# Performance work log

Hardware: AMD Instinct MI355X
Metric: run time of the kernel (lower is better)

## Reference

```python
import math
import jax, jax.numpy as jnp
import numpy as np

H = 16  # num_heads

def get_alibi_slopes(n):
    def pow2_slopes(n):
        start = 2 ** (-2 ** (-(math.log2(n) - 3)))
        return [start * start ** i for i in range(n)]
    if math.log2(n).is_integer():
        return pow2_slopes(n)
    c = 2 ** math.floor(math.log2(n))
    return pow2_slopes(c) + get_alibi_slopes(2 * c)[0::2][: n - c]

def alibi_bias(num_heads, L, dtype=jnp.float32):
    slopes = jnp.asarray(get_alibi_slopes(num_heads), dtype=dtype)  # [H]
    pos = jnp.arange(L)
    rel = (pos[None, :] - pos[:, None]).astype(dtype)               # [L, L] = x - y
    bias = slopes[:, None, None] * rel[None, :, :]                  # [H, L, L]
    causal = pos[None, :] <= pos[:, None]                           # tril mask
    return jnp.where(causal[None, :, :], bias, -jnp.inf)


def setup_inputs() -> dict:
    key = jax.random.key(0)
    ks = jax.random.split(key, 4)
    D = 1024
    B, L = 2, 2048
    s_in = 1.0 / math.sqrt(D)
    return {
        "x": jax.random.normal(ks[0], (B, L, D), dtype=jnp.float32),
        "w_in": jax.random.normal(ks[1], (D, 3 * D), dtype=jnp.float32) * s_in,
        "b_in": jnp.zeros((3 * D,), dtype=jnp.float32),
        "w_out": jax.random.normal(ks[2], (D, D), dtype=jnp.float32) * s_in,
        "b_out": jnp.zeros((D,), dtype=jnp.float32),
    }


def reference(x, w_in, b_in, w_out, b_out):
    B, L, D = x.shape
    dh = D // H
    qkv = x @ w_in + b_in                                   # [B, L, 3D]
    q, k, v = jnp.split(qkv, 3, axis=-1)
    # [B, L, D] -> [B, H, L, dh]
    def heads(t):
        return t.reshape(B, L, H, dh).transpose(0, 2, 1, 3)
    q, k, v = heads(q), heads(k), heads(v)
    scores = jnp.einsum("bhqd,bhkd->bhqk", q, k) / math.sqrt(dh)
    scores = scores + alibi_bias(H, L, scores.dtype)[None]  # [B, H, L, L]
    attn = jax.nn.softmax(scores, axis=-1)
    out = jnp.einsum("bhqk,bhkd->bhqd", attn, v)            # [B, H, L, dh]
    out = out.transpose(0, 2, 1, 3).reshape(B, L, D)
    return out @ w_out + b_out
```

## Files before the change

kernel.cpp:

```cpp
#include <hip/hip_runtime.h>
#include <stdint.h>
#include <math.h>

#define NH 16
#define DH 64
#define SEQ 2048
#define DMODEL 1024

typedef short short8 __attribute__((ext_vector_type(8)));
typedef short short4v __attribute__((ext_vector_type(4)));
typedef float f32x4 __attribute__((ext_vector_type(4)));
typedef __bf16 bf16x4 __attribute__((ext_vector_type(4)));

__device__ __forceinline__ short f2bf(float f) {
  __bf16 h = (__bf16)f;
  return __builtin_bit_cast(short, h);
}
__device__ __forceinline__ short4v cvt4(f32x4 v) {
  bf16x4 b = __builtin_convertvector(v, bf16x4);
  return __builtin_bit_cast(short4v, b);
}
__device__ __forceinline__ float fast_exp2(float x) {
#if __has_builtin(__builtin_amdgcn_exp2f)
  return __builtin_amdgcn_exp2f(x);
#else
  return exp2f(x);
#endif
}

typedef const __attribute__((address_space(1))) uint32_t* gp_t;
typedef __attribute__((address_space(3))) uint32_t* lp_t;
__device__ __forceinline__ void async16(const short* g, short* l) {
  __builtin_amdgcn_global_load_lds((gp_t)g, (lp_t)l, 16, 0, 0);
}

__device__ __forceinline__ void transpose_tile(const float* __restrict__ in,
                                               short* __restrict__ out, int R, int C,
                                               int t, int tilesX, int tid) {
  __shared__ float tile[32][33];
  const int tx = tid & 31, ty = tid >> 5;
  const int c0 = (t % tilesX) * 32, r0 = (t / tilesX) * 32;
#pragma unroll
  for (int i = 0; i < 4; ++i)
    tile[ty + i * 8][tx] = in[(size_t)(r0 + ty + i * 8) * C + c0 + tx];
  __syncthreads();
#pragma unroll
  for (int i = 0; i < 4; ++i)
    out[(size_t)(c0 + ty + i * 8) * R + r0 + tx] = f2bf(tile[tx][ty + i * 8]);
}

__global__ void k_prep(const float* __restrict__ x, short* __restrict__ xb,
                       const float* __restrict__ w_in, short* __restrict__ w_in_t,
                       const float* __restrict__ w_out, short* __restrict__ w_out_t) {
  const int tid = threadIdx.x;
  const int blk = blockIdx.x;
  if (blk < 4096) {
    const int i = blk * 256 + tid;
    f32x4 v = ((const f32x4*)x)[i];
    ((short4v*)xb)[i] = cvt4(v);
  } else if (blk < 4096 + 3072) {
    transpose_tile(w_in, w_in_t, 1024, 3072, blk - 4096, 96, tid);
  } else {
    transpose_tile(w_out, w_out_t, 1024, 1024, blk - 7168, 32, tid);
  }
}

template <int MODE>
__launch_bounds__(256, 3)
__global__ void k_gemm(const short* __restrict__ A, const short* __restrict__ Bt,
                       const float* __restrict__ bias, float* __restrict__ Cf,
                       short* __restrict__ qo, short* __restrict__ ko,
                       short* __restrict__ vo) {
  constexpr int KD = 1024;
  __shared__ __align__(16) short As[128 * 64];
  __shared__ __align__(16) short Bs[128 * 64];
  const int tid = threadIdx.x;
  const int wave = tid >> 6, lane = tid & 63;
  const int quad = lane >> 4, l16 = lane & 15;
  const int wm = wave >> 1, wn = wave & 1;
  const int tM = blockIdx.y * 128, tN = blockIdx.x * 128;

  const short* pA[4];
  const short* pB[4];
  short* lA[4];
  short* lB[4];
#pragma unroll
  for (int t = 0; t < 4; ++t) {
    const int c = t * 256 + tid;
    const int row = c >> 3, gch = (c & 7) ^ (row & 7);
    pA[t] = A + (size_t)(tM + row) * KD + gch * 8;
    pB[t] = Bt + (size_t)(tN + row) * KD + gch * 8;
    lA[t] = &As[c * 8];
    lB[t] = &Bs[c * 8];
  }

  const int sw = l16 & 7;
  const int col0 = (quad ^ sw) << 3;
  const int col1 = col0 ^ 32;

  f32x4 acc[4][4] = {};

  for (int k0 = 0; k0 < KD; k0 += 64) {
    __syncthreads();
#pragma unroll
    for (int t = 0; t < 4; ++t) {
      async16(pA[t] + k0, lA[t]);
      async16(pB[t] + k0, lB[t]);
    }
    __syncthreads();
#pragma unroll
    for (int kh = 0; kh < 2; ++kh) {
      const int col = kh ? col1 : col0;
      short8 af[4], bfr[4];
#pragma unroll
      for (int i = 0; i < 4; ++i)
        af[i] = *(const short8*)&As[(wm * 64 + i * 16 + l16) * 64 + col];
#pragma unroll
      for (int i = 0; i < 4; ++i)
        bfr[i] = *(const short8*)&Bs[(wn * 64 + i * 16 + l16) * 64 + col];
#pragma unroll
      for (int i = 0; i < 4; ++i)
#pragma unroll
        for (int j = 0; j < 4; ++j)
          acc[i][j] = __builtin_amdgcn_mfma_f32_16x16x32_bf16(af[i], bfr[j], acc[i][j], 0, 0, 0);
    }
  }

  const int rbase = tM + wm * 64 + quad * 4;
#pragma unroll
  for (int i = 0; i < 4; ++i) {
#pragma unroll
    for (int j = 0; j < 4; ++j) {
      const int col = tN + wn * 64 + j * 16 + l16;
      const float bi = bias[col];
      if (MODE == 0) {
        const int which = col >> 10;
        const int h = (col & 1023) >> 6, d = col & 63;
        if (which == 2) {
          const int row0 = rbase + i * 16;
          const int b = row0 >> 11, li0 = row0 & 2047;
          f32x4 t;
#pragma unroll
          for (int rr = 0; rr < 4; ++rr) t[rr] = acc[i][j][rr] + bi;
          *(short4v*)&vo[(((size_t)(b * NH + h)) * DH + d) * SEQ + li0] = cvt4(t);
        } else {
          short* dst = (which == 0) ? qo : ko;
#pragma unroll
          for (int rr = 0; rr < 4; ++rr) {
            const int row = rbase + i * 16 + rr;
            const int b = row >> 11, li = row & 2047;
            dst[(((size_t)(b * NH + h)) * SEQ + li) * DH + d] = f2bf(acc[i][j][rr] + bi);
          }
        }
      } else {
#pragma unroll
        for (int rr = 0; rr < 4; ++rr) {
          const int row = rbase + i * 16 + rr;
          Cf[(size_t)row * DMODEL + col] = acc[i][j][rr] + bi;
        }
      }
    }
  }
}

__launch_bounds__(256)
__global__ void k_attn(const short* __restrict__ q, const short* __restrict__ k,
                       const short* __restrict__ vt, short* __restrict__ o) {
  __shared__ __align__(16) short Ks[2][64 * 64];
  __shared__ __align__(16) short Vs[2][64 * 64];
  __shared__ __align__(16) short Ps[4][16 * 64];
  const int tid = threadIdx.x;
  const int wave = tid >> 6, lane = tid & 63;
  const int quad = lane >> 4, l16 = lane & 15;
  const int sw = l16 & 7;
  const int bx = blockIdx.x;
  const int g = bx >> 5, g0 = g & 7, sel = g >> 3;
  const int qt = (sel == 0) ? 31 - g0 : (sel == 1) ? g0 : (sel == 2) ? 23 - g0 : 8 + g0;
  const int bh = bx & 31;
  const int h = bh & (NH - 1);
  const size_t base = (size_t)bh * SEQ * DH;
  const float LOG2E = 1.44269504088896f;
  const float slope2 = exp2f(-0.5f * (float)(h + 1)) * LOG2E;
  const float scale2 = 0.125f * LOG2E;
  const float FM = 12.0f;

  const int c0i = tid, c1i = 256 + tid;
  const int r0 = c0i >> 3, ch0 = (c0i & 7) ^ (r0 & 7);
  const int r1 = c1i >> 3, ch1 = (c1i & 7) ^ (r1 & 7);
  const int qk_off0 = r0 * DH + ch0 * 8;
  const int qk_off1 = r1 * DH + ch1 * 8;
  const int v_off0 = r0 * SEQ + ch0 * 8;
  const int v_off1 = r1 * SEQ + ch1 * 8;

  const int col0 = ((quad ^ sw) << 3);
  const int col1 = col0 ^ 32;
  int psoff[4];
#pragma unroll
  for (int in = 0; in < 4; ++in)
    psoff[in] = l16 * 64 + (((2 * in + (quad >> 1)) ^ sw) << 3) + (quad & 1) * 4;
  const int qlim4 = wave * 16 + l16 - 4 * quad;

  const int q0 = qt * 64;
  const int qrow = q0 + wave * 16 + l16;
  const short* qp = q + base + (size_t)qrow * DH + quad * 8;
  const short8 qb0 = *(const short8*)qp;
  const short8 qb1 = *(const short8*)(qp + 32);

  short8 ones;
#pragma unroll
  for (int j = 0; j < 8; ++j) ones[j] = (short)0x3F80;

  f32x4 accO[4] = {};
  f32x4 accL = {};
  const float qoff = -slope2 * (float)qrow - FM + slope2 * (float)(4 * quad);
  float inoff[4];
#pragma unroll
  for (int in = 0; in < 4; ++in)
    inoff[in] = qoff + slope2 * (float)(16 * in);
  const float s64 = slope2 * 64.0f;
  float rc[4];
#pragma unroll
  for (int r = 0; r < 4; ++r) rc[r] = slope2 * (float)r;

  const short* kp = k + base;
  const short* vp = vt + base;

  async16(kp + qk_off0, &Ks[0][c0i * 8]);
  async16(kp + qk_off1, &Ks[0][c1i * 8]);
  async16(vp + v_off0, &Vs[0][c0i * 8]);
  async16(vp + v_off1, &Vs[0][c1i * 8]);
  kp += 64 * DH;
  vp += 64;
  __syncthreads();

  for (int kt = 0; kt <= qt; ++kt) {
    const int cur = kt & 1, nxt = cur ^ 1;
    if (kt < qt) {
      async16(kp + qk_off0, &Ks[nxt][c0i * 8]);
      async16(kp + qk_off1, &Ks[nxt][c1i * 8]);
      async16(vp + v_off0, &Vs[nxt][c0i * 8]);
      async16(vp + v_off1, &Vs[nxt][c1i * 8]);
      kp += 64 * DH;
      vp += 64;
    }

    f32x4 s[4];
    __builtin_amdgcn_s_setprio(1);
#pragma unroll
    for (int in = 0; in < 4; ++in) {
      const short8 ka0 = *(const short8*)&Ks[cur][(in * 16 + l16) * 64 + col0];
      const short8 ka1 = *(const short8*)&Ks[cur][(in * 16 + l16) * 64 + col1];
      f32x4 t = {};
      t = __builtin_amdgcn_mfma_f32_16x16x32_bf16(ka0, qb0, t, 0, 0, 0);
      t = __builtin_amdgcn_mfma_f32_16x16x32_bf16(ka1, qb1, t, 0, 0, 0);
      s[in] = t;
    }
    __builtin_amdgcn_s_setprio(0);

    if (kt == qt) {
#pragma unroll
      for (int in = 0; in < 4; ++in) {
        f32x4 p;
#pragma unroll
        for (int r = 0; r < 4; ++r) {
          float val = fast_exp2(fmaf(s[in][r], scale2, inoff[in] + rc[r]));
          p[r] = (16 * in + r <= qlim4) ? val : 0.f;
        }
        *(short4v*)&Ps[wave][psoff[in]] = cvt4(p);
      }
    } else {
#pragma unroll
      for (int in = 0; in < 4; ++in) {
        f32x4 p;
#pragma unroll
        for (int r = 0; r < 4; ++r)
          p[r] = fast_exp2(fmaf(s[in][r], scale2, inoff[in] + rc[r]));
        *(short4v*)&Ps[wave][psoff[in]] = cvt4(p);
      }
    }
#pragma unroll
    for (int in = 0; in < 4; ++in) inoff[in] += s64;

    const short8 pa0 = *(const short8*)&Ps[wave][l16 * 64 + col0];
    const short8 pa1 = *(const short8*)&Ps[wave][l16 * 64 + col1];
    __builtin_amdgcn_s_setprio(1);
    accL = __builtin_amdgcn_mfma_f32_16x16x32_bf16(ones, pa0, accL, 0, 0, 0);
    accL = __builtin_amdgcn_mfma_f32_16x16x32_bf16(ones, pa1, accL, 0, 0, 0);
#pragma unroll
    for (int i = 0; i < 4; ++i) {
      const short8 va0 = *(const short8*)&Vs[cur][(i * 16 + l16) * 64 + col0];
      const short8 va1 = *(const short8*)&Vs[cur][(i * 16 + l16) * 64 + col1];
      accO[i] = __builtin_amdgcn_mfma_f32_16x16x32_bf16(va0, pa0, accO[i], 0, 0, 0);
      accO[i] = __builtin_amdgcn_mfma_f32_16x16x32_bf16(va1, pa1, accO[i], 0, 0, 0);
    }
    __builtin_amdgcn_s_setprio(0);
    __syncthreads();
  }

  const float inv = 1.0f / accL[0];
  const int b = bh >> 4;
  short* ob = o + ((((size_t)b * SEQ + qrow) * NH + h) * DH + 4 * quad);
#pragma unroll
  for (int i = 0; i < 4; ++i) {
    f32x4 t;
#pragma unroll
    for (int r = 0; r < 4; ++r) t[r] = accO[i][r] * inv;
    *(short4v*)&ob[16 * i] = cvt4(t);
  }
}

extern "C" void kernel_launch(void* const* d_in, const int* in_sizes, int n_in,
                              void* d_out, int out_size, void* d_ws, size_t ws_size,
                              hipStream_t stream) {
  const float* x = (const float*)d_in[0];
  const float* w_in = (const float*)d_in[1];
  const float* b_in = (const float*)d_in[2];
  const float* w_out = (const float*)d_in[3];
  const float* b_out = (const float*)d_in[4];
  float* out = (float*)d_out;

  char* ws = (char*)d_ws;
  short* xb = (short*)(ws);
  short* w_in_t = (short*)(ws + (8u << 20));
  short* w_out_t = (short*)(ws + (14u << 20));
  short* qv = (short*)(ws + (16u << 20));
  short* kv = (short*)(ws + (24u << 20));
  short* vv = (short*)(ws + (32u << 20));
  short* ao = (short*)(ws + (40u << 20));

  k_prep<<<8192, 256, 0, stream>>>(x, xb, w_in, w_in_t, w_out, w_out_t);
  k_gemm<0><<<dim3(24, 32), 256, 0, stream>>>(xb, w_in_t, b_in, nullptr, qv, kv, vv);
  k_attn<<<1024, 256, 0, stream>>>(qv, kv, vv, ao);
  k_gemm<1><<<dim3(8, 32), 256, 0, stream>>>(ao, w_out_t, b_out, out, nullptr, nullptr, nullptr);
}
```

Measured before the change: 173.9 us.

## Load K/V fragments directly from global memory, dropping shared-memory staging

After: 252.4 us. 45.1% more time.

```diff
diff --git a/kernel.cpp b/kernel.cpp
--- a/kernel.cpp
+++ b/kernel.cpp
@@ -163,11 +163,9 @@
   }
 }
 
-__launch_bounds__(256)
+__launch_bounds__(256, 4)
 __global__ void k_attn(const short* __restrict__ q, const short* __restrict__ k,
                        const short* __restrict__ vt, short* __restrict__ o) {
-  __shared__ __align__(16) short Ks[2][64 * 64];
-  __shared__ __align__(16) short Vs[2][64 * 64];
   __shared__ __align__(16) short Ps[4][16 * 64];
   const int tid = threadIdx.x;
   const int wave = tid >> 6, lane = tid & 63;
@@ -184,14 +182,6 @@
   const float scale2 = 0.125f * LOG2E;
   const float FM = 12.0f;
 
-  const int c0i = tid, c1i = 256 + tid;
-  const int r0 = c0i >> 3, ch0 = (c0i & 7) ^ (r0 & 7);
-  const int r1 = c1i >> 3, ch1 = (c1i & 7) ^ (r1 & 7);
-  const int qk_off0 = r0 * DH + ch0 * 8;
-  const int qk_off1 = r1 * DH + ch1 * 8;
-  const int v_off0 = r0 * SEQ + ch0 * 8;
-  const int v_off1 = r1 * SEQ + ch1 * 8;
-
   const int col0 = ((quad ^ sw) << 3);
   const int col1 = col0 ^ 32;
   int psoff[4];
@@ -206,6 +196,9 @@
   const short8 qb0 = *(const short8*)qp;
   const short8 qb1 = *(const short8*)(qp + 32);
 
+  const short* kfrag = k + base + (size_t)l16 * DH + quad * 8;
+  const short* vfrag = vt + base + (size_t)l16 * SEQ + quad * 8;
+
   short8 ones;
 #pragma unroll
   for (int j = 0; j < 8; ++j) ones[j] = (short)0x3F80;
@@ -222,40 +215,35 @@
 #pragma unroll
   for (int r = 0; r < 4; ++r) rc[r] = slope2 * (float)r;
 
-  const short* kp = k + base;
-  const short* vp = vt + base;
-
-  async16(kp + qk_off0, &Ks[0][c0i * 8]);
-  async16(kp + qk_off1, &Ks[0][c1i * 8]);
-  async16(vp + v_off0, &Vs[0][c0i * 8]);
-  async16(vp + v_off1, &Vs[0][c1i * 8]);
-  kp += 64 * DH;
-  vp += 64;
-  __syncthreads();
-
   for (int kt = 0; kt <= qt; ++kt) {
-    const int cur = kt & 1, nxt = cur ^ 1;
-    if (kt < qt) {
-      async16(kp + qk_off0, &Ks[nxt][c0i * 8]);
-      async16(kp + qk_off1, &Ks[nxt][c1i * 8]);
-      async16(vp + v_off0, &Vs[nxt][c0i * 8]);
-      async16(vp + v_off1, &Vs[nxt][c1i * 8]);
-      kp += 64 * DH;
-      vp += 64;
+    const int koff = kt * 64;
+
+    short8 ka0[4], ka1[4];
+#pragma unroll
+    for (int in = 0; in < 4; ++in) {
+      const short* kp = kfrag + (size_t)(koff + in * 16) * DH;
+      ka0[in] = *(const short8*)kp;
+      ka1[in] = *(const short8*)(kp + 32);
     }
 
     f32x4 s[4];
     __builtin_amdgcn_s_setprio(1);
 #pragma unroll
     for (int in = 0; in < 4; ++in) {
-      const short8 ka0 = *(const short8*)&Ks[cur][(in * 16 + l16) * 64 + col0];
-      const short8 ka1 = *(const short8*)&Ks[cur][(in * 16 + l16) * 64 + col1];
       f32x4 t = {};
-      t = __builtin_amdgcn_mfma_f32_16x16x32_bf16(ka0, qb0, t, 0, 0, 0);
-      t = __builtin_amdgcn_mfma_f32_16x16x32_bf16(ka1, qb1, t, 0, 0, 0);
+      t = __builtin_amdgcn_mfma_f32_16x16x32_bf16(ka0[in], qb0, t, 0, 0, 0);
+      t = __builtin_amdgcn_mfma_f32_16x16x32_bf16(ka1[in], qb1, t, 0, 0, 0);
       s[in] = t;
     }
     __builtin_amdgcn_s_setprio(0);
+
+    short8 va0[4], va1[4];
+#pragma unroll
+    for (int i = 0; i < 4; ++i) {
+      const short* vp = vfrag + (size_t)(i * 16) * SEQ + koff;
+      va0[i] = *(const short8*)vp;
+      va1[i] = *(const short8*)(vp + 32);
+    }
 
     if (kt == qt) {
 #pragma unroll
@@ -288,13 +276,10 @@
     accL = __builtin_amdgcn_mfma_f32_16x16x32_bf16(ones, pa1, accL, 0, 0, 0);
 #pragma unroll
     for (int i = 0; i < 4; ++i) {
-      const short8 va0 = *(const short8*)&Vs[cur][(i * 16 + l16) * 64 + col0];
-      const short8 va1 = *(const short8*)&Vs[cur][(i * 16 + l16) * 64 + col1];
-      accO[i] = __builtin_amdgcn_mfma_f32_16x16x32_bf16(va0, pa0, accO[i], 0, 0, 0);
-      accO[i] = __builtin_amdgcn_mfma_f32_16x16x32_bf16(va1, pa1, accO[i], 0, 0, 0);
+      accO[i] = __builtin_amdgcn_mfma_f32_16x16x32_bf16(va0[i], pa0, accO[i], 0, 0, 0);
+      accO[i] = __builtin_amdgcn_mfma_f32_16x16x32_bf16(va1[i], pa1, accO[i], 0, 0, 0);
     }
     __builtin_amdgcn_s_setprio(0);
-    __syncthreads();
   }
 
   const float inv = 1.0f / accL[0];
```

## Software-pipeline attention loop: defer PV MFMAs one iteration behind QK

Applied to the files above, without the earlier changes.

Measured after the change: 193.9 us. 11.5% more time.

```diff
diff --git a/kernel.cpp b/kernel.cpp
--- a/kernel.cpp
+++ b/kernel.cpp
@@ -163,7 +163,7 @@
   }
 }
 
-__launch_bounds__(256)
+__launch_bounds__(256, 4)
 __global__ void k_attn(const short* __restrict__ q, const short* __restrict__ k,
                        const short* __restrict__ vt, short* __restrict__ o) {
   __shared__ __align__(16) short Ks[2][64 * 64];
@@ -233,6 +233,9 @@
   vp += 64;
   __syncthreads();
 
+  short8 paA, paB;
+  short8 var0[4], var1[4];
+
   for (int kt = 0; kt <= qt; ++kt) {
     const int cur = kt & 1, nxt = cur ^ 1;
     if (kt < qt) {
@@ -244,18 +247,38 @@
       vp += 64;
     }
 
+    short8 ka0[4], ka1[4];
+#pragma unroll
+    for (int in = 0; in < 4; ++in) {
+      ka0[in] = *(const short8*)&Ks[cur][(in * 16 + l16) * 64 + col0];
+      ka1[in] = *(const short8*)&Ks[cur][(in * 16 + l16) * 64 + col1];
+    }
     f32x4 s[4];
     __builtin_amdgcn_s_setprio(1);
 #pragma unroll
     for (int in = 0; in < 4; ++in) {
-      const short8 ka0 = *(const short8*)&Ks[cur][(in * 16 + l16) * 64 + col0];
-      const short8 ka1 = *(const short8*)&Ks[cur][(in * 16 + l16) * 64 + col1];
       f32x4 t = {};
-      t = __builtin_amdgcn_mfma_f32_16x16x32_bf16(ka0, qb0, t, 0, 0, 0);
-      t = __builtin_amdgcn_mfma_f32_16x16x32_bf16(ka1, qb1, t, 0, 0, 0);
+      t = __builtin_amdgcn_mfma_f32_16x16x32_bf16(ka0[in], qb0, t, 0, 0, 0);
+      t = __builtin_amdgcn_mfma_f32_16x16x32_bf16(ka1[in], qb1, t, 0, 0, 0);
       s[in] = t;
     }
+
+    if (kt > 0) {
+      accL = __builtin_amdgcn_mfma_f32_16x16x32_bf16(ones, paA, accL, 0, 0, 0);
+      accL = __builtin_amdgcn_mfma_f32_16x16x32_bf16(ones, paB, accL, 0, 0, 0);
+#pragma unroll
+      for (int i = 0; i < 4; ++i) {
+        accO[i] = __builtin_amdgcn_mfma_f32_16x16x32_bf16(var0[i], paA, accO[i], 0, 0, 0);
+        accO[i] = __builtin_amdgcn_mfma_f32_16x16x32_bf16(var1[i], paB, accO[i], 0, 0, 0);
+      }
+    }
     __builtin_amdgcn_s_setprio(0);
+
+#pragma unroll
+    for (int i = 0; i < 4; ++i) {
+      var0[i] = *(const short8*)&Vs[cur][(i * 16 + l16) * 64 + col0];
+      var1[i] = *(const short8*)&Vs[cur][(i * 16 + l16) * 64 + col1];
+    }
 
     if (kt == qt) {
 #pragma unroll
@@ -281,21 +304,21 @@
 #pragma unroll
     for (int in = 0; in < 4; ++in) inoff[in] += s64;
 
-    const short8 pa0 = *(const short8*)&Ps[wave][l16 * 64 + col0];
-    const short8 pa1 = *(const short8*)&Ps[wave][l16 * 64 + col1];
-    __builtin_amdgcn_s_setprio(1);
-    accL = __builtin_amdgcn_mfma_f32_16x16x32_bf16(ones, pa0, accL, 0, 0, 0);
-    accL = __builtin_amdgcn_mfma_f32_16x16x32_bf16(ones, pa1, accL, 0, 0, 0);
-#pragma unroll
-    for (int i = 0; i < 4; ++i) {
-      const short8 va0 = *(const short8*)&Vs[cur][(i * 16 + l16) * 64 + col0];
-      const short8 va1 = *(const short8*)&Vs[cur][(i * 16 + l16) * 64 + col1];
-      accO[i] = __builtin_amdgcn_mfma_f32_16x16x32_bf16(va0, pa0, accO[i], 0, 0, 0);
-      accO[i] = __builtin_amdgcn_mfma_f32_16x16x32_bf16(va1, pa1, accO[i], 0, 0, 0);
-    }
-    __builtin_amdgcn_s_setprio(0);
+    paA = *(const short8*)&Ps[wave][l16 * 64 + col0];
+    paB = *(const short8*)&Ps[wave][l16 * 64 + col1];
+
     __syncthreads();
   }
+
+  __builtin_amdgcn_s_setprio(1);
+  accL = __builtin_amdgcn_mfma_f32_16x16x32_bf16(ones, paA, accL, 0, 0, 0);
+  accL = __builtin_amdgcn_mfma_f32_16x16x32_bf16(ones, paB, accL, 0, 0, 0);
+#pragma unroll
+  for (int i = 0; i < 4; ++i) {
+    accO[i] = __builtin_amdgcn_mfma_f32_16x16x32_bf16(var0[i], paA, accO[i], 0, 0, 0);
+    accO[i] = __builtin_amdgcn_mfma_f32_16x16x32_bf16(var1[i], paB, accO[i], 0, 0, 0);
+  }
+  __builtin_amdgcn_s_setprio(0);
 
   const float inv = 1.0f / accL[0];
   const int b = bh >> 4;
```
